# Optimization experiments

Hardware: AMD Instinct MI355X
Metric: run time of the kernel (lower is better)

## Reference

```python
import jax, jax.numpy as jnp
import numpy as np

LOG_2PI = float(np.log(2.0 * np.pi))
MASK_SCORE = -1.0e15


def setup_inputs() -> dict:
    key = jax.random.key(0)
    k1, k2, k3, k4 = jax.random.split(key, 4)
    B, H, D, T = 32, 600, 512, 2400
    encoder_outputs = jax.random.normal(k1, (B, H, D), dtype=jnp.float32)
    # per-phoneme durations in frames (float, as the torch code casts via cumsum().float())
    durations = jax.random.randint(k2, (B, H), 0, 8).astype(jnp.float32)
    # per-phoneme Gaussian variances; keep strictly positive for log(vars)
    vars_ = jax.random.uniform(k3, (B, H), dtype=jnp.float32) * 0.9 + 0.1
    input_lengths = jax.random.randint(k4, (B,), 1, H, dtype=jnp.int32)
    return {
        "encoder_outputs": encoder_outputs,
        "durations": durations,
        "vars": vars_,
        "input_lengths": input_lengths,
        "frame_length": T,
    }


def reference(encoder_outputs, durations, vars, input_lengths, frame_length):
    # encoder_outputs: [B, H, D]; durations, vars: [B, H]; input_lengths: [B]
    B, H, D = encoder_outputs.shape
    # Gaussian centers: cumulative duration minus half the phoneme's own duration
    c = jnp.cumsum(durations, axis=1) - 0.5 * durations            # [B, H]
    t = jnp.arange(frame_length, dtype=jnp.float32)                 # [T]
    # log N(t; c, vars): [B, H, T]
    diff = t[None, None, :] - c[:, :, None]
    w_t = -0.5 * (LOG_2PI + jnp.log(vars)[:, :, None] + diff * diff / vars[:, :, None])
    # mask out padded phoneme positions (h >= input_length)
    pad_mask = jnp.arange(H)[None, :] >= input_lengths[:, None]     # [B, H]
    w_t = jnp.where(pad_mask[:, :, None], MASK_SCORE, w_t)
    # softmax over the phoneme (hidden) axis
    w_t = jax.nn.softmax(w_t, axis=1)                                # [B, H, T]
    # upsample: [B, T, H] @ [B, H, D] -> [B, T, D]
    return jnp.einsum("bht,bhd->btd", w_t, encoder_outputs)
```

## Files before the change

kernel.cpp:

```cpp
#include <hip/hip_runtime.h>
#include <hip/hip_bf16.h>

using f32x4   = __attribute__((ext_vector_type(4))) float;
using short8  = __attribute__((ext_vector_type(8))) short;
using short4v = __attribute__((ext_vector_type(4))) short;

#define LOG2_2PI 2.6514961294723187f
#define L2E_HALF 0.7213475204444817f
#define HP2 640

__device__ __forceinline__ short bf16bits(float x) {
  unsigned u = __builtin_bit_cast(unsigned, x);
  u = (u + 0x7FFFu + ((u >> 16) & 1u)) >> 16;
  return (short)u;
}
__device__ __forceinline__ float bf16round(float x) {
  unsigned u = __builtin_bit_cast(unsigned, x);
  u = ((u + 0x7FFFu + ((u >> 16) & 1u)) >> 16) << 16;
  return __builtin_bit_cast(float, u);
}

__global__ void prep_kernel(const float* __restrict__ dur,
                            const float* __restrict__ vars,
                            const int* __restrict__ lens,
                            f32x4* __restrict__ pk, float* __restrict__ aux,
                            int H) {
  const int b = blockIdx.x;
  const int l = threadIdx.x;
  const int L = lens[b];
  float run = 0.f, prevD = 0.f;
  float Gmax = 0.f, qMin = 1e30f, qMax = 0.f, bMin = 1e30f, bMax = -1e30f;
  for (int h0 = 0; h0 < HP2; h0 += 64) {
    const int h = h0 + l;
    const float d = (h < H) ? dur[(size_t)b * H + h] : 0.f;
    float x = d;
#pragma unroll
    for (int off = 1; off < 64; off <<= 1) {
      float y = __shfl_up(x, off);
      if (l >= off) x += y;
    }
    float dp = __shfl_up(d, 1);
    if (l == 0) dp = prevD;
    f32x4 e = (f32x4){0.f, 0.f, -1e30f, 0.f};
    if (h < H) {
      const float v = vars[(size_t)b * H + h];
      const float q = L2E_HALF / v;
      const float bc = -0.5f * (LOG2_2PI + __builtin_amdgcn_logf(v));
      e[0] = run + x - 0.5f * d;
      e[1] = q;
      e[2] = (h < L) ? bc : -1e30f;
      if (h < L) {
        qMin = fminf(qMin, q); qMax = fmaxf(qMax, q);
        bMin = fminf(bMin, bc); bMax = fmaxf(bMax, bc);
        if (h >= 1) Gmax = fmaxf(Gmax, 0.5f * (d + dp));
      }
    }
    pk[(size_t)b * HP2 + h] = e;
    prevD = __shfl(d, 63);
    run += __shfl(x, 63);
  }
#pragma unroll
  for (int off = 1; off < 64; off <<= 1) {
    qMin = fminf(qMin, __shfl_xor(qMin, off));
    qMax = fmaxf(qMax, __shfl_xor(qMax, off));
    bMin = fminf(bMin, __shfl_xor(bMin, off));
    bMax = fmaxf(bMax, __shfl_xor(bMax, off));
    Gmax = fmaxf(Gmax, __shfl_xor(Gmax, off));
  }
  if (l == 0) {
    float* ax = aux + b * 8;
    ax[0] = Gmax; ax[1] = qMin; ax[2] = qMax; ax[3] = bMin; ax[4] = bMax;
  }
}

__global__ void win_kernel(const f32x4* __restrict__ pk,
                           const float* __restrict__ aux,
                           const int* __restrict__ lens,
                           int* __restrict__ win, int T, int TT) {
  const int b = blockIdx.x;
  const int L = lens[b];
  const float Gmax = aux[b * 8 + 0], qMn = aux[b * 8 + 1], qMx = aux[b * 8 + 2];
  const float bMn  = aux[b * 8 + 3], bMx = aux[b * 8 + 4];
  const f32x4* pc = pk + (size_t)b * HP2;
  const float c0 = pc[0][0], cL = pc[L - 1][0];
  for (int tile = threadIdx.x; tile < TT; tile += blockDim.x) {
    const float tLo = (float)(tile * 32);
    const float tHi = (float)(min(tile * 32 + 31, T - 1));
    const float D0 = fmaxf(0.5f * Gmax, fmaxf(fmaxf(c0 - tLo, tHi - cL), 0.f));
    const float Wr = __fsqrt_rn(((bMx - bMn) + 65.f + qMx * D0 * D0) / qMn);
    int lo = 0, hi = L;
    const float thLo = tLo - Wr;
    while (lo < hi) { const int mid = (lo + hi) >> 1; if (pc[mid][0] < thLo) lo = mid + 1; else hi = mid; }
    int hLo = lo;
    int lo2 = hLo, hi2 = L;
    const float thHi = tHi + Wr;
    while (lo2 < hi2) { const int mid = (lo2 + hi2) >> 1; if (pc[mid][0] <= thHi) lo2 = mid + 1; else hi2 = mid; }
    int hHi = lo2;
    if (hHi <= hLo) { hLo = max(hLo - 1, 0); hHi = min(hLo + 2, L); }
    win[(b * TT + tile) * 2 + 0] = hLo >> 6;
    win[(b * TT + tile) * 2 + 1] = (hHi + 63) >> 6;
  }
}

__global__ void transpose_kernel(const float* __restrict__ enc,
                                 short* __restrict__ encT,
                                 const int* __restrict__ lens,
                                 int H, int D) {
  __shared__ short sT[64][66];
  const int b  = blockIdx.z;
  const int h0 = blockIdx.y * 64;
  const int d0 = blockIdx.x * 64;
  const int Lpad = (lens[b] + 63) & ~63;
  if (h0 >= Lpad) return;
  const int tid = threadIdx.x;

  const int dc = (tid & 15) * 4;
  const int hr = tid >> 4;
#pragma unroll
  for (int ps = 0; ps < 4; ++ps) {
    const int hh = hr + ps * 16;
    const int h  = h0 + hh;
    f32x4 v = (h < H) ? *(const f32x4*)&enc[((size_t)b * H + h) * D + d0 + dc]
                      : (f32x4){0.f, 0.f, 0.f, 0.f};
#pragma unroll
    for (int j = 0; j < 4; ++j) sT[dc + j][hh] = bf16bits(v[j]);
  }
  __syncthreads();

  const int tx4 = (tid & 15) * 4;
  const int ty2 = tid >> 4;
#pragma unroll
  for (int i = 0; i < 4; ++i) {
    const int d = d0 + ty2 + i * 16;
    short4v v;
#pragma unroll
    for (int j = 0; j < 4; ++j) v[j] = sT[ty2 + i * 16][tx4 + j];
    *(short4v*)&encT[((size_t)b * D + d) * HP2 + h0 + tx4] = v;
  }
}

__launch_bounds__(256, 3)
__global__ void gup_kernel(const short* __restrict__ encT,
                           const f32x4* __restrict__ pk,
                           const int* __restrict__ win,
                           float* __restrict__ out,
                           int T, int TT) {
  constexpr int D  = 512;
  constexpr int AS = 72;

  __shared__ __align__(16) float sc[HP2], sq[HP2], sb[HP2];
  __shared__ float sden[32];
  __shared__ short sA[2][32 * AS];

  const int tid   = threadIdx.x;
  const int b     = blockIdx.y;
  const int tIdx  = blockIdx.x >> 1;
  const int t0    = tIdx * 32;
  const int dbase = (blockIdx.x & 1) * 256;

  const int cLo = win[(b * TT + tIdx) * 2 + 0];
  const int cHi = win[(b * TT + tIdx) * 2 + 1];
  const int base = cLo * 64;
  const int nC   = cHi - cLo;
  const int W64  = nC * 64;

  for (int i = tid; i < W64; i += 256) {
    const f32x4 v = pk[(size_t)b * HP2 + base + i];
    sc[i] = v[0]; sq[i] = v[1]; sb[i] = v[2];
  }
  __syncthreads();

  const int tfA = tid >> 3;
  const int hs8 = tid & 7;
  const float tA = (float)(t0 + tfA);
  float mA = -1e30f;
  for (int h4 = hs8 * 4; h4 < W64; h4 += 32) {
    const f32x4 cv = *(const f32x4*)&sc[h4];
    const f32x4 qv = *(const f32x4*)&sq[h4];
    const f32x4 bv = *(const f32x4*)&sb[h4];
#pragma unroll
    for (int j = 0; j < 4; ++j) {
      const float dd = tA - cv[j];
      mA = fmaxf(mA, fmaf(-dd * dd, qv[j], bv[j]));
    }
  }
  mA = fmaxf(mA, __shfl_xor(mA, 1));
  mA = fmaxf(mA, __shfl_xor(mA, 2));
  mA = fmaxf(mA, __shfl_xor(mA, 4));

  const int lane = tid & 63;
  const int wv   = tid >> 6;
  const int l15  = lane & 15;
  const int lq   = lane >> 4;

  f32x4 acc[2][4];
#pragma unroll
  for (int i = 0; i < 2; ++i)
#pragma unroll
    for (int j = 0; j < 4; ++j) acc[i][j] = (f32x4){0.f, 0.f, 0.f, 0.f};

  const int k8 = hs8 * 8;
  float denAcc = 0.f;
  const short* bp = encT + ((size_t)b * D + dbase + wv * 64 + l15) * HP2 + base + lq * 8;

  int p = 0;
  for (int cc = 0; cc < nC; ++cc) {
    const int hb = cc * 64 + k8;
    const f32x4 cv0 = *(const f32x4*)&sc[hb];
    const f32x4 qv0 = *(const f32x4*)&sq[hb];
    const f32x4 bv0 = *(const f32x4*)&sb[hb];
    const f32x4 cv1 = *(const f32x4*)&sc[hb + 4];
    const f32x4 qv1 = *(const f32x4*)&sq[hb + 4];
    const f32x4 bv1 = *(const f32x4*)&sb[hb + 4];
    short8 w;
    float denAdd = 0.f, pmax = 0.f;
#pragma unroll
    for (int j = 0; j < 4; ++j) {
      const float dd = tA - cv0[j];
      const float pv = __builtin_amdgcn_exp2f(fmaf(-dd * dd, qv0[j], bv0[j]) - mA);
      w[j] = bf16bits(pv);
      denAdd += bf16round(pv);
      pmax = fmaxf(pmax, pv);
    }
#pragma unroll
    for (int j = 0; j < 4; ++j) {
      const float dd = tA - cv1[j];
      const float pv = __builtin_amdgcn_exp2f(fmaf(-dd * dd, qv1[j], bv1[j]) - mA);
      w[4 + j] = bf16bits(pv);
      denAdd += bf16round(pv);
      pmax = fmaxf(pmax, pv);
    }

    if (!__syncthreads_or(pmax > 1e-20f)) continue;

    denAcc += denAdd;
    *(short8*)&sA[p][tfA * AS + k8] = w;
    __syncthreads();

#pragma unroll
    for (int kh = 0; kh < 2; ++kh) {
      short8 bfv[4];
#pragma unroll
      for (int nt = 0; nt < 4; ++nt)
        bfv[nt] = *(const short8*)(bp + (size_t)nt * 16 * HP2 + cc * 64 + kh * 32);
      short8 af[2];
#pragma unroll
      for (int mt = 0; mt < 2; ++mt)
        af[mt] = *(short8*)&sA[p][(mt * 16 + l15) * AS + kh * 32 + lq * 8];
#pragma unroll
      for (int mt = 0; mt < 2; ++mt)
#pragma unroll
        for (int nt = 0; nt < 4; ++nt)
          acc[mt][nt] = __builtin_amdgcn_mfma_f32_16x16x32_bf16(bfv[nt], af[mt], acc[mt][nt], 0, 0, 0);
    }
    p ^= 1;
  }

  {
    float dsum = denAcc;
    dsum += __shfl_xor(dsum, 1);
    dsum += __shfl_xor(dsum, 2);
    dsum += __shfl_xor(dsum, 4);
    if (hs8 == 0) sden[tfA] = dsum;
  }
  __syncthreads();

#pragma unroll
  for (int mt = 0; mt < 2; ++mt) {
    const int tg = t0 + mt * 16 + l15;
    const float inv = 1.0f / sden[mt * 16 + l15];
    if (tg < T) {
#pragma unroll
      for (int nt = 0; nt < 4; ++nt) {
        f32x4 o;
#pragma unroll
        for (int i = 0; i < 4; ++i) o[i] = acc[mt][nt][i] * inv;
        *(f32x4*)&out[((size_t)b * T + tg) * D + dbase + wv * 64 + nt * 16 + lq * 4] = o;
      }
    }
  }
}

extern "C" void kernel_launch(void* const* d_in, const int* in_sizes, int n_in,
                              void* d_out, int out_size, void* d_ws, size_t ws_size,
                              hipStream_t stream) {
  const float* enc  = (const float*)d_in[0];
  const float* dur  = (const float*)d_in[1];
  const float* vars = (const float*)d_in[2];
  const int*   lens = (const int*)d_in[3];

  const int B = in_sizes[3];
  const int H = in_sizes[1] / B;
  const int D = in_sizes[0] / in_sizes[1];
  const int T = out_size / (B * D);
  const int TT = (T + 31) / 32;
  (void)n_in; (void)ws_size;

  f32x4* pk  = (f32x4*)d_ws;
  float* aux = (float*)(pk + (size_t)B * HP2);
  int*   wn  = (int*)(aux + 8 * (size_t)B);
  short* encT = (short*)(wn + (size_t)B * TT * 2);

  prep_kernel<<<B, 64, 0, stream>>>(dur, vars, lens, pk, aux, H);

  win_kernel<<<B, 128, 0, stream>>>(pk, aux, lens, wn, T, TT);

  dim3 tgrid(D / 64, HP2 / 64, B);
  transpose_kernel<<<tgrid, 256, 0, stream>>>(enc, encT, lens, H, D);

  dim3 grid(TT * 2, B);
  gup_kernel<<<grid, 256, 0, stream>>>(encT, pk, wn, (float*)d_out, T, TT);
}
```

Baseline: 76.11 us.

## Merge D-halves into one 512-thread block per time tile

Each block now covers the full 512-wide D for its 32-frame tile with 8 waves, instead of two 256-thread blocks each covering half of D. The softmax weights, max and denominators are computed once per tile rather than twice, halving the exp/weight work and the per-tile parameter loads. Each thread now computes 4 weights instead of 8. The trade-offs are half as many blocks, larger blocks with more barrier participants, and a new occupancy target in the launch bounds.

```diff
diff --git a/kernel.cpp b/kernel.cpp
--- a/kernel.cpp
+++ b/kernel.cpp
@@ -139,7 +139,7 @@
   }
 }
 
-__launch_bounds__(256, 3)
+__launch_bounds__(512, 4)
 __global__ void gup_kernel(const short* __restrict__ encT,
                            const f32x4* __restrict__ pk,
                            const int* __restrict__ win,
@@ -152,11 +152,10 @@
   __shared__ float sden[32];
   __shared__ short sA[2][32 * AS];
 
-  const int tid   = threadIdx.x;
-  const int b     = blockIdx.y;
-  const int tIdx  = blockIdx.x >> 1;
-  const int t0    = tIdx * 32;
-  const int dbase = (blockIdx.x & 1) * 256;
+  const int tid  = threadIdx.x;
+  const int b    = blockIdx.y;
+  const int tIdx = blockIdx.x;
+  const int t0   = tIdx * 32;
 
   const int cLo = win[(b * TT + tIdx) * 2 + 0];
   const int cHi = win[(b * TT + tIdx) * 2 + 1];
@@ -164,17 +163,18 @@
   const int nC   = cHi - cLo;
   const int W64  = nC * 64;
 
-  for (int i = tid; i < W64; i += 256) {
+  for (int i = tid; i < W64; i += 512) {
     const f32x4 v = pk[(size_t)b * HP2 + base + i];
     sc[i] = v[0]; sq[i] = v[1]; sb[i] = v[2];
   }
   __syncthreads();
 
-  const int tfA = tid >> 3;
-  const int hs8 = tid & 7;
+  const int tfA  = tid >> 4;
+  const int hs16 = tid & 15;
+  const int k4   = hs16 * 4;
   const float tA = (float)(t0 + tfA);
   float mA = -1e30f;
-  for (int h4 = hs8 * 4; h4 < W64; h4 += 32) {
+  for (int h4 = k4; h4 < W64; h4 += 64) {
     const f32x4 cv = *(const f32x4*)&sc[h4];
     const f32x4 qv = *(const f32x4*)&sq[h4];
     const f32x4 bv = *(const f32x4*)&sb[h4];
@@ -187,6 +187,7 @@
   mA = fmaxf(mA, __shfl_xor(mA, 1));
   mA = fmaxf(mA, __shfl_xor(mA, 2));
   mA = fmaxf(mA, __shfl_xor(mA, 4));
+  mA = fmaxf(mA, __shfl_xor(mA, 8));
 
   const int lane = tid & 63;
   const int wv   = tid >> 6;
@@ -199,20 +200,16 @@
 #pragma unroll
     for (int j = 0; j < 4; ++j) acc[i][j] = (f32x4){0.f, 0.f, 0.f, 0.f};
 
-  const int k8 = hs8 * 8;
   float denAcc = 0.f;
-  const short* bp = encT + ((size_t)b * D + dbase + wv * 64 + l15) * HP2 + base + lq * 8;
+  const short* bp = encT + ((size_t)b * D + wv * 64 + l15) * HP2 + base + lq * 8;
 
   int p = 0;
   for (int cc = 0; cc < nC; ++cc) {
-    const int hb = cc * 64 + k8;
+    const int hb = cc * 64 + k4;
     const f32x4 cv0 = *(const f32x4*)&sc[hb];
     const f32x4 qv0 = *(const f32x4*)&sq[hb];
     const f32x4 bv0 = *(const f32x4*)&sb[hb];
-    const f32x4 cv1 = *(const f32x4*)&sc[hb + 4];
-    const f32x4 qv1 = *(const f32x4*)&sq[hb + 4];
-    const f32x4 bv1 = *(const f32x4*)&sb[hb + 4];
-    short8 w;
+    short4v w;
     float denAdd = 0.f, pmax = 0.f;
 #pragma unroll
     for (int j = 0; j < 4; ++j) {
@@ -222,19 +219,11 @@
       denAdd += bf16round(pv);
       pmax = fmaxf(pmax, pv);
     }
-#pragma unroll
-    for (int j = 0; j < 4; ++j) {
-      const float dd = tA - cv1[j];
-      const float pv = __builtin_amdgcn_exp2f(fmaf(-dd * dd, qv1[j], bv1[j]) - mA);
-      w[4 + j] = bf16bits(pv);
-      denAdd += bf16round(pv);
-      pmax = fmaxf(pmax, pv);
-    }
 
     if (!__syncthreads_or(pmax > 1e-20f)) continue;
 
     denAcc += denAdd;
-    *(short8*)&sA[p][tfA * AS + k8] = w;
+    *(short4v*)&sA[p][tfA * AS + k4] = w;
     __syncthreads();
 
 #pragma unroll
@@ -261,7 +250,8 @@
     dsum += __shfl_xor(dsum, 1);
     dsum += __shfl_xor(dsum, 2);
     dsum += __shfl_xor(dsum, 4);
-    if (hs8 == 0) sden[tfA] = dsum;
+    dsum += __shfl_xor(dsum, 8);
+    if (hs16 == 0) sden[tfA] = dsum;
   }
   __syncthreads();
 
@@ -275,7 +265,7 @@
         f32x4 o;
 #pragma unroll
         for (int i = 0; i < 4; ++i) o[i] = acc[mt][nt][i] * inv;
-        *(f32x4*)&out[((size_t)b * T + tg) * D + dbase + wv * 64 + nt * 16 + lq * 4] = o;
+        *(f32x4*)&out[((size_t)b * T + tg) * D + wv * 64 + nt * 16 + lq * 4] = o;
       }
     }
   }
@@ -308,6 +298,6 @@
   dim3 tgrid(D / 64, HP2 / 64, B);
   transpose_kernel<<<tgrid, 256, 0, stream>>>(enc, encT, lens, H, D);
 
-  dim3 grid(TT * 2, B);
-  gup_kernel<<<grid, 256, 0, stream>>>(encT, pk, wn, (float*)d_out, T, TT);
-}
+  dim3 grid(TT, B);
+  gup_kernel<<<grid, 512, 0, stream>>>(encT, pk, wn, (float*)d_out, T, TT);
+}
```

After: 81.17 us. +6.6%, slower.
